# Kernel optimization log

Measured on AMD Instinct MI355X. Metric: run time of the kernel, lower is better.

The kernel has to match this reference:

```python
import jax, jax.numpy as jnp
import numpy as np

PRECISION = 2.0 ** 24  # ctx._precision stand-in; factor = sqrt(precision)
SF_CONST = 48.0


def setup_inputs() -> dict:
    key = jax.random.key(0)
    k1, k2, k3 = jax.random.split(key, 3)
    x = jax.random.normal(k1, (16, 128, 128, 128), dtype=jnp.float32)  # NCHW
    W = jax.random.normal(k2, (256, 128, 3, 3), dtype=jnp.float32) * 0.05  # OIHW
    b = jax.random.normal(k3, (256,), dtype=jnp.float32) * 0.1
    return {"x": x, "W": W, "b": b}


def reference(x, W, b):
    # --- quantize() (standard, non-mixture path) ---
    N = float(np.prod(W.shape[1:]))           # in_ch * kh * kw = 1152
    factor = np.sqrt(PRECISION)               # sqrt(ctx._precision)
    sf = np.sqrt(SF_CONST / N)
    w_sum = jnp.sum(jnp.abs(W), axis=(1, 2, 3))          # [O]
    w_sum = jnp.where(w_sum == 0, 1.0, w_sum)
    fw = (factor / sf - np.sqrt(N / 12.0) * 5.0) / w_sum  # [O]
    Wq = jnp.round(W * fw[:, None, None, None])

    # --- forward int-quantized conv ---
    x_max = jnp.max(jnp.abs(x))
    fx = jnp.where(x_max > 0, (factor * sf - 0.5) / x_max, 1.0)
    xq = jnp.round(fx * x)
    y = jax.lax.conv_general_dilated(
        xq, Wq,
        window_strides=(1, 1),
        padding=((1, 1), (1, 1)),
        dimension_numbers=("NCHW", "OIHW", "NCHW"),
    )
    # dequantize per output channel, then fused float bias add
    y = y / (fx * fw[:, None, None]) + b[:, None, None]
    # Activation (ReLU); BN disabled, dropout disabled in this config
    return jax.nn.relu(y)
```

## Files before the change

kernel.cpp:

```cpp
#include <hip/hip_runtime.h>
#include <math.h>


#define FW_NUM 20017.23017802413f
#define FX_NUM 835.5924988699913f
#define WQA_OFF 2048
#define WQB_OFF (640 * 1024)
#define ZP_OFF  (1536 * 1024)
#define XQ_OFF  (2 * 1024 * 1024)
#define XQ_BYTES 67108864ull

#define CK  16
#define CKP 24
#define JW  130

typedef _Float16 half8 __attribute__((ext_vector_type(8)));
typedef _Float16 half4 __attribute__((ext_vector_type(4)));
typedef float floatx16 __attribute__((ext_vector_type(16)));

__device__ __forceinline__ void gl_lds16(const void* g, void* s) {
    __builtin_amdgcn_global_load_lds((const __attribute__((address_space(1))) void*)g,
                                     (__attribute__((address_space(3))) void*)s, 16, 0, 0);
}

__global__ void xmax_kernel(const float* __restrict__ x, unsigned int* wsu, int n4) {
    int tid = blockIdx.x * blockDim.x + threadIdx.x;
    int stride = gridDim.x * blockDim.x;
    const float4* x4 = (const float4*)x;
    float m = 0.f;
    for (int i = tid; i < n4; i += stride) {
        float4 v = x4[i];
        m = fmaxf(m, fmaxf(fmaxf(fabsf(v.x), fabsf(v.y)), fmaxf(fabsf(v.z), fabsf(v.w))));
    }
    #pragma unroll
    for (int off = 32; off >= 1; off >>= 1)
        m = fmaxf(m, __shfl_down(m, off, 64));
    __shared__ float sm[4];
    if ((threadIdx.x & 63) == 0) sm[threadIdx.x >> 6] = m;
    __syncthreads();
    if (threadIdx.x == 0) {
        m = fmaxf(fmaxf(sm[0], sm[1]), fmaxf(sm[2], sm[3]));
        atomicMax(wsu, __float_as_uint(m));
    }
}

__global__ void wq_kernel(const float* __restrict__ W, float* wsf, int big) {
    int o = blockIdx.x;
    int t = threadIdx.x;
    const float* wrow = W + o * 1152;
    float wv[9];
    float s = 0.f;
    #pragma unroll
    for (int k = 0; k < 9; k++) { wv[k] = wrow[t * 9 + k]; s += fabsf(wv[k]); }
    #pragma unroll
    for (int off = 32; off >= 1; off >>= 1) s += __shfl_down(s, off, 64);
    __shared__ float sred[2];
    __shared__ float sfw;
    if ((t & 63) == 0) sred[t >> 6] = s;
    __syncthreads();
    if (t == 0) {
        float wsum = sred[0] + sred[1];
        if (wsum == 0.f) wsum = 1.f;
        float fw = FW_NUM / wsum;
        wsf[64 + o] = fw;
        sfw = fw;
    }
    __syncthreads();
    float fw = sfw;
    _Float16* wqa = (_Float16*)((char*)wsf + WQA_OFF);
    _Float16* wqb = (_Float16*)((char*)wsf + WQB_OFF);
    int oswz = (o & ~3) | ((o & 3) ^ ((o >> 3) & 3));
    int qflip = (o >> 2) & 1;
    #pragma unroll
    for (int k = 0; k < 9; k++) {
        _Float16 hv = (_Float16)rintf(wv[k] * fw);
        wqa[(o * 9 + k) * 128 + t] = hv;
        if (big) {
            int q = (t >> 3) & 1;
            int qswz = q ^ qflip;
            wqb[(((t >> 4) * 9 + k) * 256 + oswz) * 16 + qswz * 8 + (t & 7)] = hv;
        }
    }
}

__global__ void quantx_kernel(const float* __restrict__ x, const float* __restrict__ wsf,
                              _Float16* __restrict__ xq) {
    int bid = blockIdx.x;
    int h  = bid & 127;
    int cc = (bid >> 7) & 7;
    int n  = bid >> 10;
    float xmax = __uint_as_float(((const unsigned int*)wsf)[0]);
    float fx = xmax > 0.f ? FX_NUM / xmax : 1.0f;
    int w = threadIdx.x;
    const float* xp = x + ((size_t)(n * 128 + cc * 16) * 128 + h) * 128 + w;
    half8 v0, v1;
    #pragma unroll
    for (int ci = 0; ci < 8; ci++)  v0[ci] = (_Float16)rintf(fx * xp[(size_t)ci * 16384]);
    #pragma unroll
    for (int ci = 8; ci < 16; ci++) v1[ci - 8] = (_Float16)rintf(fx * xp[(size_t)ci * 16384]);
    _Float16* op = xq + ((size_t)bid * 128 + w) * 16;
    *(half8*)op = v0;
    *(half8*)(op + 8) = v1;
}

__global__ __launch_bounds__(256, 2) void conv_main(const _Float16* __restrict__ xq,
                                                    const float* __restrict__ bias,
                                                    const float* __restrict__ wsf,
                                                    float* __restrict__ out) {
    __shared__ __align__(16) _Float16 xs[2][10240];
    __shared__ __align__(16) _Float16 wl[2][9728];
    __shared__ float sc[64], bz[64];

    float xmax = __uint_as_float(((const unsigned int*)wsf)[0]);
    float fx = xmax > 0.f ? FX_NUM / xmax : 1.0f;

    int bx0 = blockIdx.x;
    int bx = (bx0 & 7) * 256 + (bx0 >> 3);
    int o0 = (bx & 3) << 6;
    int w0 = ((bx >> 2) & 3) << 5;
    int h0 = ((bx >> 4) & 7) << 4;
    int n  = bx >> 7;

    int tid = threadIdx.x;
    int lane = tid & 63;
    int wv = tid >> 6;
    int m32 = lane & 31;
    int q2 = lane >> 5;

    const char* wsb = (const char*)wsf;

    int xcol[3];
    #pragma unroll
    for (int kw = 0; kw < 3; ++kw) {
        int j = m32 + kw;
        xcol[kw] = (j * 32 + q2 * 16) ^ ((((j) >> 2) & 7) << 4);
    }
    int wcol = (m32 * 32 + q2 * 16) ^ (((m32 >> 2) & 7) << 4);

    int goff[10];
    int gstr[10];
    #pragma unroll
    for (int k = 0; k < 10; ++k) {
        int s = wv + 4 * k;
        int off, str;
        if (s < 20) {
            int slot = s * 64 + lane;
            int r = (slot * 241) >> 14;
            int spi = slot - r * 68;
            int u = spi ^ ((spi >> 3) & 7);
            int j = u >> 1, q = u & 1;
            int h = h0 + r - 1, w = w0 + j - 1;
            bool ok = (slot < 1224) && (h >= 0) && (h < 128) && (w >= 0) && (w < 128);
            if (ok) {
                off = XQ_OFF + n * 4194304 + (h * 128 + w) * 32 + q * 16;
                str = 524288;
            } else {
                off = ZP_OFF + lane * 16;
                str = 0;
            }
        } else if (s < 38) {
            int t2 = s - 20, tap = t2 >> 1, g = t2 & 1;
            off = WQB_OFF + (tap * 256 + o0) * 32 + g * 1024 + lane * 16;
            str = 73728;
        } else {
            off = ZP_OFF + lane * 16;
            str = 0;
        }
        goff[k] = off;
        gstr[k] = str;
    }

    auto stage = [&](int tb) {
        #pragma unroll
        for (int k = 0; k < 10; ++k) {
            int s = wv + 4 * k;
            char* dst;
            if (s < 20)      dst = (char*)&xs[tb][0] + s * 1024;
            else if (s < 38) dst = (char*)&wl[tb][0] + (s - 20) * 1024;
            else             dst = (char*)&wl[tb][0] + 18 * 1024;
            gl_lds16(wsb + goff[k], dst);
            goff[k] += gstr[k];
        }
    };

    if (tid < 64) {
        float fwv = wsf[64 + o0 + tid];
        sc[tid] = 1.0f / (fx * fwv);
        bz[tid] = bias[o0 + tid];
    }
    __syncthreads();

    floatx16 acc[2][4];
    #pragma unroll
    for (int a1 = 0; a1 < 2; a1++)
        #pragma unroll
        for (int a2 = 0; a2 < 4; a2++)
            #pragma unroll
            for (int e = 0; e < 16; e++) acc[a1][a2][e] = 0.f;

    stage(0);

    for (int cc = 0; cc < 8; ++cc) {
        int cb = cc & 1;
        __builtin_amdgcn_s_barrier();
        if (cc < 7) {
            stage(cb ^ 1);
            asm volatile("s_waitcnt vmcnt(10)" ::: "memory");
        } else {
            asm volatile("s_waitcnt vmcnt(0)" ::: "memory");
        }
        __builtin_amdgcn_s_barrier();

        const char* xb = (const char*)&xs[cb][0] + wv * (4 * 1088);
        const char* wb = (const char*)&wl[cb][0];
        #pragma unroll
        for (int kw = 0; kw < 3; ++kw) {
            half8 xf[6];
            #pragma unroll
            for (int srow = 0; srow < 6; ++srow)
                xf[srow] = *(const half8*)(xb + srow * 1088 + xcol[kw]);
            #pragma unroll
            for (int kh = 0; kh < 3; ++kh) {
                const char* wp = wb + (kh * 3 + kw) * 2048 + wcol;
                half8 wf0 = *(const half8*)wp;
                half8 wf1 = *(const half8*)(wp + 1024);
                __builtin_amdgcn_s_setprio(1);
                #pragma unroll
                for (int p = 0; p < 4; ++p) {
                    acc[0][p] = __builtin_amdgcn_mfma_f32_32x32x16_f16(wf0, xf[p + kh], acc[0][p], 0, 0, 0);
                    acc[1][p] = __builtin_amdgcn_mfma_f32_32x32x16_f16(wf1, xf[p + kh], acc[1][p], 0, 0, 0);
                }
                __builtin_amdgcn_s_setprio(0);
            }
        }
    }

    #pragma unroll
    for (int ot = 0; ot < 2; ++ot) {
        #pragma unroll
        for (int e = 0; e < 16; ++e) {
            int o_loc = ot * 32 + (e & 3) + 8 * (e >> 2) + 4 * q2;
            float scale = sc[o_loc];
            float bv = bz[o_loc];
            #pragma unroll
            for (int p = 0; p < 4; ++p) {
                int h = h0 + wv * 4 + p;
                float v = fmaxf(fmaf(acc[ot][p][e], scale, bv), 0.f);
                out[(((size_t)(n * 256 + o0 + o_loc)) * 128 + h) * 128 + w0 + m32] = v;
            }
        }
    }
}

__global__ __launch_bounds__(256, 2) void conv_fallback(const float* __restrict__ x,
                                                        const float* __restrict__ bias,
                                                        const float* __restrict__ wsf,
                                                        float* __restrict__ out) {
    __shared__ __align__(16) _Float16 xs[6 * JW * CKP];
    __shared__ __align__(16) _Float16 wlds[9 * 64 * CKP];

    const unsigned int* wsu = (const unsigned int*)wsf;
    float xmax = __uint_as_float(wsu[0]);
    float fx = xmax > 0.f ? FX_NUM / xmax : 1.0f;

    int bx = blockIdx.x;
    int n  = bx >> 5;
    int h0 = (bx & 31) << 2;
    int o0 = blockIdx.y << 6;

    int tid  = threadIdx.x;
    int lane = tid & 63;
    int wave = tid >> 6;
    int m32  = lane & 31;
    int q2   = lane >> 5;

    const _Float16* wq16 = (const _Float16*)((const char*)wsf + WQA_OFF);
    const float* xn = x + (size_t)n * (128 * 128 * 128);

    floatx16 acc[4][2];
    #pragma unroll
    for (int mt = 0; mt < 4; mt++)
        #pragma unroll
        for (int nt = 0; nt < 2; nt++)
            #pragma unroll
            for (int e = 0; e < 16; e++) acc[mt][nt][e] = 0.f;

    if (tid < 192) {
        int r = tid >> 5;
        int s = tid & 31;
        int c = s & 15;
        int j = (s >> 4) ? (JW - 1) : 0;
        xs[(r * JW + j) * CKP + c] = (_Float16)0.f;
    }

    for (int c0 = 0; c0 < 128; c0 += CK) {
        __syncthreads();
        #pragma unroll
        for (int it = 0; it < 12; ++it) {
            int idx = tid + it * 256;
            int j  = (idx & 127) + 1;
            int c4 = (idx >> 7) & 3;
            int r  = idx >> 9;
            int h  = h0 + r - 1;
            float v0 = 0.f, v1 = 0.f, v2 = 0.f, v3 = 0.f;
            if (h >= 0 && h < 128) {
                const float* xp = xn + (size_t)(c0 + c4 * 4) * 16384 + h * 128 + (j - 1);
                v0 = xp[0]; v1 = xp[16384]; v2 = xp[32768]; v3 = xp[49152];
            }
            half4 hv;
            hv[0] = (_Float16)rintf(fx * v0);
            hv[1] = (_Float16)rintf(fx * v1);
            hv[2] = (_Float16)rintf(fx * v2);
            hv[3] = (_Float16)rintf(fx * v3);
            *(half4*)&xs[(r * JW + j) * CKP + c4 * 4] = hv;
        }
        #pragma unroll
        for (int it = 0; it < 5; ++it) {
            int idx = tid + it * 256;
            if (idx < 1152) {
                int o   = idx / 18;
                int rem = idx - o * 18;
                int tap = rem >> 1;
                int g   = rem & 1;
                half8 v = *(const half8*)(wq16 + ((size_t)(o0 + o) * 9 + tap) * 128 + c0 + g * 8);
                *(half8*)&wlds[(tap * 64 + o) * CKP + g * 8] = v;
            }
        }
        __syncthreads();

        const _Float16* xbase = &xs[(wave * JW + m32) * CKP + q2 * 8];
        const _Float16* wbase = &wlds[m32 * CKP + q2 * 8];
        #pragma unroll
        for (int kh = 0; kh < 3; ++kh) {
            #pragma unroll
            for (int kw = 0; kw < 3; ++kw) {
                int tap = kh * 3 + kw;
                half8 b0 = *(const half8*)(wbase + (tap * 64 +  0) * CKP);
                half8 b1 = *(const half8*)(wbase + (tap * 64 + 32) * CKP);
                #pragma unroll
                for (int mt = 0; mt < 4; ++mt) {
                    half8 a = *(const half8*)(xbase + (kh * JW + kw + mt * 32) * CKP);
                    acc[mt][0] = __builtin_amdgcn_mfma_f32_32x32x16_f16(a, b0, acc[mt][0], 0, 0, 0);
                    acc[mt][1] = __builtin_amdgcn_mfma_f32_32x32x16_f16(a, b1, acc[mt][1], 0, 0, 0);
                }
            }
        }
    }

    int h = h0 + wave;
    #pragma unroll
    for (int nt = 0; nt < 2; ++nt) {
        int o = o0 + nt * 32 + m32;
        float fwv = wsf[64 + o];
        float scale = 1.0f / (fx * fwv);
        float bv = bias[o];
        float* op = out + (((size_t)n * 256 + o) * 128 + h) * 128;
        #pragma unroll
        for (int mt = 0; mt < 4; ++mt) {
            #pragma unroll
            for (int g = 0; g < 4; ++g) {
                int w = mt * 32 + 8 * g + 4 * q2;
                float4 r;
                r.x = fmaxf(fmaf(acc[mt][nt][4 * g + 0], scale, bv), 0.f);
                r.y = fmaxf(fmaf(acc[mt][nt][4 * g + 1], scale, bv), 0.f);
                r.z = fmaxf(fmaf(acc[mt][nt][4 * g + 2], scale, bv), 0.f);
                r.w = fmaxf(fmaf(acc[mt][nt][4 * g + 3], scale, bv), 0.f);
                *(float4*)(op + w) = r;
            }
        }
    }
}

extern "C" void kernel_launch(void* const* d_in, const int* in_sizes, int n_in,
                              void* d_out, int out_size, void* d_ws, size_t ws_size,
                              hipStream_t stream) {
    const float* x = (const float*)d_in[0];
    const float* W = (const float*)d_in[1];
    const float* b = (const float*)d_in[2];
    float* out = (float*)d_out;
    float* wsf = (float*)d_ws;

    int big = (ws_size >= (size_t)XQ_OFF + XQ_BYTES) ? 1 : 0;

    hipMemsetAsync(d_ws, 0, 256, stream);
    if (big)
        hipMemsetAsync((char*)d_ws + ZP_OFF, 0, 2048, stream);

    xmax_kernel<<<1024, 256, 0, stream>>>(x, (unsigned int*)d_ws, (16 * 128 * 128 * 128) / 4);
    wq_kernel<<<256, 128, 0, stream>>>(W, wsf, big);

    if (big) {
        _Float16* xq = (_Float16*)((char*)d_ws + XQ_OFF);
        quantx_kernel<<<16 * 8 * 128, 128, 0, stream>>>(x, wsf, xq);
        conv_main<<<2048, 256, 0, stream>>>(xq, b, wsf, out);
    } else {
        dim3 grid(512, 4);
        conv_fallback<<<grid, 256, 0, stream>>>(x, b, wsf, out);
    }
}
```

Baseline: 497.5 us.

## Read conv weights directly from global memory and halve output-channel tile

```diff
diff --git a/kernel.cpp b/kernel.cpp
--- a/kernel.cpp
+++ b/kernel.cpp
@@ -69,17 +69,12 @@
     float fw = sfw;
     _Float16* wqa = (_Float16*)((char*)wsf + WQA_OFF);
     _Float16* wqb = (_Float16*)((char*)wsf + WQB_OFF);
-    int oswz = (o & ~3) | ((o & 3) ^ ((o >> 3) & 3));
-    int qflip = (o >> 2) & 1;
     #pragma unroll
     for (int k = 0; k < 9; k++) {
         _Float16 hv = (_Float16)rintf(wv[k] * fw);
         wqa[(o * 9 + k) * 128 + t] = hv;
-        if (big) {
-            int q = (t >> 3) & 1;
-            int qswz = q ^ qflip;
-            wqb[(((t >> 4) * 9 + k) * 256 + oswz) * 16 + qswz * 8 + (t & 7)] = hv;
-        }
+        if (big)
+            wqb[(((t >> 4) * 9 + k) * 256 + o) * 16 + (t & 15)] = hv;
     }
 }
 
@@ -103,23 +98,22 @@
     *(half8*)(op + 8) = v1;
 }
 
-__global__ __launch_bounds__(256, 2) void conv_main(const _Float16* __restrict__ xq,
+__global__ __launch_bounds__(256, 3) void conv_main(const _Float16* __restrict__ xq,
                                                     const float* __restrict__ bias,
                                                     const float* __restrict__ wsf,
                                                     float* __restrict__ out) {
     __shared__ __align__(16) _Float16 xs[2][10240];
-    __shared__ __align__(16) _Float16 wl[2][9728];
-    __shared__ float sc[64], bz[64];
+    __shared__ float sc[32], bz[32];
 
     float xmax = __uint_as_float(((const unsigned int*)wsf)[0]);
     float fx = xmax > 0.f ? FX_NUM / xmax : 1.0f;
 
     int bx0 = blockIdx.x;
-    int bx = (bx0 & 7) * 256 + (bx0 >> 3);
-    int o0 = (bx & 3) << 6;
-    int w0 = ((bx >> 2) & 3) << 5;
-    int h0 = ((bx >> 4) & 7) << 4;
-    int n  = bx >> 7;
+    int bx = (bx0 & 7) * 512 + (bx0 >> 3);
+    int o0 = (bx & 7) << 5;
+    int w0 = ((bx >> 3) & 3) << 5;
+    int h0 = ((bx >> 5) & 7) << 4;
+    int n  = bx >> 8;
 
     int tid = threadIdx.x;
     int lane = tid & 63;
@@ -129,74 +123,45 @@
 
     const char* wsb = (const char*)wsf;
 
-    int xcol[3];
-    #pragma unroll
-    for (int kw = 0; kw < 3; ++kw) {
-        int j = m32 + kw;
-        xcol[kw] = (j * 32 + q2 * 16) ^ ((((j) >> 2) & 7) << 4);
-    }
-    int wcol = (m32 * 32 + q2 * 16) ^ (((m32 >> 2) & 7) << 4);
-
-    int goff[10];
-    int gstr[10];
-    #pragma unroll
-    for (int k = 0; k < 10; ++k) {
+    int goff[5];
+    int gstr[5];
+    #pragma unroll
+    for (int k = 0; k < 5; ++k) {
         int s = wv + 4 * k;
-        int off, str;
-        if (s < 20) {
-            int slot = s * 64 + lane;
-            int r = (slot * 241) >> 14;
-            int spi = slot - r * 68;
-            int u = spi ^ ((spi >> 3) & 7);
-            int j = u >> 1, q = u & 1;
-            int h = h0 + r - 1, w = w0 + j - 1;
-            bool ok = (slot < 1224) && (h >= 0) && (h < 128) && (w >= 0) && (w < 128);
-            if (ok) {
-                off = XQ_OFF + n * 4194304 + (h * 128 + w) * 32 + q * 16;
-                str = 524288;
-            } else {
-                off = ZP_OFF + lane * 16;
-                str = 0;
-            }
-        } else if (s < 38) {
-            int t2 = s - 20, tap = t2 >> 1, g = t2 & 1;
-            off = WQB_OFF + (tap * 256 + o0) * 32 + g * 1024 + lane * 16;
-            str = 73728;
+        int slot = s * 64 + lane;
+        int r = (slot * 241) >> 14;
+        int spi = slot - r * 68;
+        int h = h0 + r - 1;
+        int w = w0 + (spi >> 1) - 1;
+        bool ok = (slot < 1224) && (h >= 0) && (h < 128) && (w >= 0) && (w < 128);
+        if (ok) {
+            goff[k] = XQ_OFF + n * 4194304 + (h * 128 + w) * 32 + (spi & 1) * 16;
+            gstr[k] = 524288;
         } else {
-            off = ZP_OFF + lane * 16;
-            str = 0;
-        }
-        goff[k] = off;
-        gstr[k] = str;
-    }
-
+            goff[k] = ZP_OFF + lane * 16;
+            gstr[k] = 0;
+        }
+    }
     auto stage = [&](int tb) {
         #pragma unroll
-        for (int k = 0; k < 10; ++k) {
+        for (int k = 0; k < 5; ++k) {
             int s = wv + 4 * k;
-            char* dst;
-            if (s < 20)      dst = (char*)&xs[tb][0] + s * 1024;
-            else if (s < 38) dst = (char*)&wl[tb][0] + (s - 20) * 1024;
-            else             dst = (char*)&wl[tb][0] + 18 * 1024;
-            gl_lds16(wsb + goff[k], dst);
+            gl_lds16(wsb + goff[k], (char*)&xs[tb][0] + s * 1024);
             goff[k] += gstr[k];
         }
     };
 
-    if (tid < 64) {
+    if (tid < 32) {
         float fwv = wsf[64 + o0 + tid];
         sc[tid] = 1.0f / (fx * fwv);
         bz[tid] = bias[o0 + tid];
     }
-    __syncthreads();
-
-    floatx16 acc[2][4];
-    #pragma unroll
-    for (int a1 = 0; a1 < 2; a1++)
-        #pragma unroll
-        for (int a2 = 0; a2 < 4; a2++)
-            #pragma unroll
-            for (int e = 0; e < 16; e++) acc[a1][a2][e] = 0.f;
+
+    floatx16 acc[4];
+    #pragma unroll
+    for (int p = 0; p < 4; ++p)
+        #pragma unroll
+        for (int e = 0; e < 16; ++e) acc[p][e] = 0.f;
 
     stage(0);
 
@@ -205,49 +170,55 @@
         __builtin_amdgcn_s_barrier();
         if (cc < 7) {
             stage(cb ^ 1);
-            asm volatile("s_waitcnt vmcnt(10)" ::: "memory");
+            asm volatile("s_waitcnt vmcnt(5)" ::: "memory");
         } else {
             asm volatile("s_waitcnt vmcnt(0)" ::: "memory");
         }
         __builtin_amdgcn_s_barrier();
 
         const char* xb = (const char*)&xs[cb][0] + wv * (4 * 1088);
-        const char* wb = (const char*)&wl[cb][0];
+        const char* wq_c = wsb + WQB_OFF + (size_t)cc * 73728 + (o0 + m32) * 32 + q2 * 16;
+
+        half8 wfA[3], wfB[3];
+        #pragma unroll
+        for (int kh = 0; kh < 3; ++kh)
+            wfA[kh] = *(const half8*)(wq_c + (kh * 3 + 0) * 8192);
+
         #pragma unroll
         for (int kw = 0; kw < 3; ++kw) {
             half8 xf[6];
             #pragma unroll
             for (int srow = 0; srow < 6; ++srow)
-                xf[srow] = *(const half8*)(xb + srow * 1088 + xcol[kw]);
+                xf[srow] = *(const half8*)(xb + srow * 1088 + (m32 + kw) * 32 + q2 * 16);
+            if (kw < 2) {
+                #pragma unroll
+                for (int kh = 0; kh < 3; ++kh) {
+                    if (kw & 1) wfA[kh] = *(const half8*)(wq_c + (kh * 3 + kw + 1) * 8192);
+                    else        wfB[kh] = *(const half8*)(wq_c + (kh * 3 + kw + 1) * 8192);
+                }
+            }
+            __builtin_amdgcn_s_setprio(1);
             #pragma unroll
             for (int kh = 0; kh < 3; ++kh) {
-                const char* wp = wb + (kh * 3 + kw) * 2048 + wcol;
-                half8 wf0 = *(const half8*)wp;
-                half8 wf1 = *(const half8*)(wp + 1024);
-                __builtin_amdgcn_s_setprio(1);
+                half8 wcur = (kw & 1) ? wfB[kh] : wfA[kh];
                 #pragma unroll
-                for (int p = 0; p < 4; ++p) {
-                    acc[0][p] = __builtin_amdgcn_mfma_f32_32x32x16_f16(wf0, xf[p + kh], acc[0][p], 0, 0, 0);
-                    acc[1][p] = __builtin_amdgcn_mfma_f32_32x32x16_f16(wf1, xf[p + kh], acc[1][p], 0, 0, 0);
-                }
-                __builtin_amdgcn_s_setprio(0);
-            }
-        }
-    }
-
-    #pragma unroll
-    for (int ot = 0; ot < 2; ++ot) {
-        #pragma unroll
-        for (int e = 0; e < 16; ++e) {
-            int o_loc = ot * 32 + (e & 3) + 8 * (e >> 2) + 4 * q2;
-            float scale = sc[o_loc];
-            float bv = bz[o_loc];
-            #pragma unroll
-            for (int p = 0; p < 4; ++p) {
-                int h = h0 + wv * 4 + p;
-                float v = fmaxf(fmaf(acc[ot][p][e], scale, bv), 0.f);
-                out[(((size_t)(n * 256 + o0 + o_loc)) * 128 + h) * 128 + w0 + m32] = v;
-            }
+                for (int p = 0; p < 4; ++p)
+                    acc[p] = __builtin_amdgcn_mfma_f32_32x32x16_f16(wcur, xf[p + kh], acc[p], 0, 0, 0);
+            }
+            __builtin_amdgcn_s_setprio(0);
+        }
+    }
+
+    #pragma unroll
+    for (int e = 0; e < 16; ++e) {
+        int o_loc = (e & 3) + 8 * (e >> 2) + 4 * q2;
+        float scale = sc[o_loc];
+        float bv = bz[o_loc];
+        #pragma unroll
+        for (int p = 0; p < 4; ++p) {
+            int h = h0 + wv * 4 + p;
+            float v = fmaxf(fmaf(acc[p][e], scale, bv), 0.f);
+            out[(((size_t)(n * 256 + o0 + o_loc)) * 128 + h) * 128 + w0 + m32] = v;
         }
     }
 }
@@ -392,7 +363,7 @@
     if (big) {
         _Float16* xq = (_Float16*)((char*)d_ws + XQ_OFF);
         quantx_kernel<<<16 * 8 * 128, 128, 0, stream>>>(x, wsf, xq);
-        conv_main<<<2048, 256, 0, stream>>>(xq, b, wsf, out);
+        conv_main<<<4096, 256, 0, stream>>>(xq, b, wsf, out);
     } else {
         dim3 grid(512, 4);
         conv_fallback<<<grid, 256, 0, stream>>>(x, b, wsf, out);
```

Measured after the change: 509.6 us. 1.02x slower.
